# Performance work log

Measured on AMD Instinct MI355X. Metric: run time of the kernel, lower is better.

The kernel has to match this reference:

```python
import jax, jax.numpy as jnp
import numpy as np

N_NODES = 100000
N_EDGES = 1600000
N_GRAPHS = 1024
IN_CH = 64
HID = 32
H4, H2 = HID * 4, HID * 2


def _glorot(key, shape):
    fan_in, fan_out = shape[0], shape[1]
    lim = (6.0 / (fan_in + fan_out)) ** 0.5
    return jax.random.uniform(key, shape, jnp.float32, -lim, lim)


def setup_inputs() -> dict:
    key = jax.random.key(0)
    ks = jax.random.split(key, 32)
    inp = {
        "x": jax.random.normal(ks[0], (N_NODES, IN_CH), jnp.float32),
        "edge_index": jax.random.randint(ks[1], (2, N_EDGES), 0, N_NODES, jnp.int64),
        "batch": jnp.sort(jax.random.randint(ks[2], (N_NODES,), 0, N_GRAPHS, jnp.int64)),
    }
    dims = [(IN_CH, H4), (H4, H2), (H2, H2), (H2, H2)]
    for i, (di, do) in enumerate(dims, 1):
        inp[f"c{i}_wl"] = _glorot(ks[3 * i], (di, do))
        inp[f"c{i}_bl"] = jnp.zeros((do,), jnp.float32)
        inp[f"c{i}_wr"] = _glorot(ks[3 * i + 1], (di, do))
    lin_dims = [(H2, H2), (H2, HID), (HID, HID), (HID, 1)]
    for i, (di, do) in enumerate(lin_dims, 1):
        inp[f"lin{i}_w"] = _glorot(ks[15 + 2 * i], (di, do))
        inp[f"lin{i}_b"] = jnp.zeros((do,), jnp.float32)
    return inp


def _sage(x, src, dst, wl, bl, wr):
    # mean-aggregate neighbor (source) features at target nodes
    agg = jax.ops.segment_sum(x[src], dst, num_segments=N_NODES)
    deg = jax.ops.segment_sum(jnp.ones((src.shape[0],), x.dtype), dst, num_segments=N_NODES)
    agg = agg / jnp.maximum(deg, 1.0)[:, None]
    return agg @ wl + bl + x @ wr


def reference(x, edge_index, batch,
              c1_wl, c1_bl, c1_wr, c2_wl, c2_bl, c2_wr,
              c3_wl, c3_bl, c3_wr, c4_wl, c4_bl, c4_wr,
              lin1_w, lin1_b, lin2_w, lin2_b, lin3_w, lin3_b, lin4_w, lin4_b):
    src, dst = edge_index[0], edge_index[1]
    h = jax.nn.relu(_sage(x, src, dst, c1_wl, c1_bl, c1_wr))
    h = jax.nn.relu(_sage(h, src, dst, c2_wl, c2_bl, c2_wr))
    h = jax.nn.relu(_sage(h, src, dst, c3_wl, c3_bl, c3_wr))
    h = jax.nn.relu(_sage(h, src, dst, c4_wl, c4_bl, c4_wr))
    # global mean pool over graphs
    gsum = jax.ops.segment_sum(h, batch, num_segments=N_GRAPHS)
    gcnt = jax.ops.segment_sum(jnp.ones((h.shape[0],), h.dtype), batch, num_segments=N_GRAPHS)
    g = gsum / jnp.maximum(gcnt, 1.0)[:, None]
    g = jax.nn.relu(g @ lin1_w + lin1_b)
    g = jax.nn.relu(g @ lin2_w + lin2_b)
    g = jax.nn.relu(g @ lin3_w + lin3_b)
    out = (g @ lin4_w + lin4_b).squeeze(1)  # [N_GRAPHS]
    return out
```

## Files before the change

kernel.cpp:

```cpp
#include <hip/hip_runtime.h>

#define NN 100000
#define NE 1600000
#define NG 1024
#define CPAD 4
#define MAXDEG 64

#define GB_COUNT 6250
#define GB_Z     1563
#define GB_CVT   3125
#define GB_BND   5
#define GB_PREP  320
#define GB_ODD   (GB_Z + GB_CVT + GB_BND + GB_PREP)
#define GB_SETUP 12504

typedef __attribute__((ext_vector_type(8))) short bf16x8;
typedef __attribute__((ext_vector_type(4))) float f32x4;

__device__ __forceinline__ unsigned f2bf1(float f) {
  union { float f; unsigned u; } v; v.f = f;
  return (v.u + 0x7fffu + ((v.u >> 16) & 1u)) >> 16;
}
__device__ __forceinline__ unsigned packbf2(float a, float b) {
  return f2bf1(a) | (f2bf1(b) << 16);
}
__device__ __forceinline__ float bflo(unsigned u) {
  union { unsigned u; float f; } v; v.u = u << 16; return v.f;
}
__device__ __forceinline__ float bfhi(unsigned u) {
  union { unsigned u; float f; } v; v.u = u & 0xffff0000u; return v.f;
}
__device__ __forceinline__ float bfs(unsigned short s) {
  union { unsigned u; float f; } v; v.u = ((unsigned)s) << 16; return v.f;
}

#define ACC16(A, P0, P1)                                              \
  A[0] += bflo(P0.x); A[1] += bfhi(P0.x);                             \
  A[2] += bflo(P0.y); A[3] += bfhi(P0.y);                             \
  A[4] += bflo(P0.z); A[5] += bfhi(P0.z);                             \
  A[6] += bflo(P0.w); A[7] += bfhi(P0.w);                             \
  A[8] += bflo(P1.x); A[9] += bfhi(P1.x);                             \
  A[10] += bflo(P1.y); A[11] += bfhi(P1.y);                           \
  A[12] += bflo(P1.z); A[13] += bfhi(P1.z);                           \
  A[14] += bflo(P1.w); A[15] += bfhi(P1.w);

#define ACC8(A, V)                                                    \
  A[0] += bflo(V.x); A[1] += bfhi(V.x);                               \
  A[2] += bflo(V.y); A[3] += bfhi(V.y);                               \
  A[4] += bflo(V.z); A[5] += bfhi(V.z);                               \
  A[6] += bflo(V.w); A[7] += bfhi(V.w);

__global__ __launch_bounds__(256) void k_prepz(const float* __restrict__ c1wr,
                                               unsigned short* __restrict__ pLZ) {
  int e = blockIdx.x * 256 + threadIdx.x;
  if (e >= 64 * 128) return;
  int k = e >> 7, n = e & 127;
  int t = k >> 5, kq = (k >> 3) & 3, j = k & 7;
  int n0 = n >> 4, nl = n & 15;
  pLZ[((((n0 * 2 + t) * 64) + (kq * 16 + nl)) << 3) + j] =
      (unsigned short)f2bf1(c1wr[k * 128 + n]);
}

__global__ __launch_bounds__(256) void k_setup(
    const int* __restrict__ src, const int* __restrict__ dst,
    int* __restrict__ cnt, int* __restrict__ csr,
    const float* __restrict__ X, unsigned short* __restrict__ Xb,
    const int* __restrict__ batch, int* __restrict__ gstart,
    const unsigned short* __restrict__ pLZ, const float* __restrict__ c1bl,
    unsigned short* __restrict__ ZZ,
    const float* __restrict__ c1wl, const float* __restrict__ c1wr,
    const float* __restrict__ c2wl, const float* __restrict__ c2wr,
    const float* __restrict__ c3wl, const float* __restrict__ c3wr,
    const float* __restrict__ c4wl, const float* __restrict__ c4wr,
    unsigned short* __restrict__ pL1, unsigned short* __restrict__ pL2a,
    unsigned short* __restrict__ pL2b, unsigned short* __restrict__ pL3,
    unsigned short* __restrict__ pL4) {
  __shared__ __align__(16) char smem[64 * 66 * 4];
  int b = blockIdx.x, tid = threadIdx.x;
  int g = b >> 3, i = b & 7;

  if ((g & 1) == 0) {
    int cb = (g >> 1) * 8 + i;
    if (cb >= GB_COUNT) return;
    int e = cb * 256 + tid;
    int d = dst[e];
    int s = src[e];
    int r = atomicAdd(&cnt[(size_t)d * CPAD], 1);
    if (r < MAXDEG) csr[d * MAXDEG + r] = s;
    return;
  }
  int ob = (g >> 1) * 8 + i;
  if (ob >= GB_ODD) return;

  if (ob < GB_Z) {
    unsigned short* sA = (unsigned short*)smem;
    float* sC = (float*)smem;
    const int m0 = ob * 64;
#pragma unroll
    for (int l = 0; l < 2; ++l) {
      int c = tid + l * 256;
      int m = c >> 3, k8 = c & 7;
      int row = m0 + m;
      uint4 o = make_uint4(0, 0, 0, 0);
      if (row < NN) {
        const float4* xp = (const float4*)(X + (size_t)row * 64 + k8 * 8);
        float4 p0 = xp[0], p1 = xp[1];
        o.x = packbf2(p0.x, p0.y); o.y = packbf2(p0.z, p0.w);
        o.z = packbf2(p1.x, p1.y); o.w = packbf2(p1.z, p1.w);
      }
      int wv = m >> 4, mr = m & 15, t = k8 >> 2, kq = k8 & 3;
      ((uint4*)sA)[(wv * 2 + t) * 64 + kq * 16 + mr] = o;
    }
    __syncthreads();
    const int w = tid >> 6, L = tid & 63;
    const bf16x8* Af = (const bf16x8*)sA;
    const bf16x8* Bf = (const bf16x8*)pLZ;
    f32x4 acc[8];
#pragma unroll
    for (int i2 = 0; i2 < 8; ++i2)
#pragma unroll
      for (int j = 0; j < 4; ++j) acc[i2][j] = 0.f;
#pragma unroll
    for (int t = 0; t < 2; ++t) {
      bf16x8 afr = Af[(w * 2 + t) * 64 + L];
#pragma unroll
      for (int n0 = 0; n0 < 8; ++n0) {
        bf16x8 bfr = Bf[(n0 * 2 + t) * 64 + L];
        acc[n0] = __builtin_amdgcn_mfma_f32_16x16x32_bf16(afr, bfr, acc[n0], 0, 0, 0);
      }
    }
    int rg = L >> 4, cl = L & 15;
#pragma unroll
    for (int half = 0; half < 2; ++half) {
      __syncthreads();
#pragma unroll
      for (int n0 = 0; n0 < 4; ++n0)
#pragma unroll
        for (int r = 0; r < 4; ++r)
          sC[(w * 16 + rg * 4 + r) * 66 + n0 * 16 + cl] = acc[half * 4 + n0][r];
      __syncthreads();
#pragma unroll
      for (int it = 0; it < 2; ++it) {
        int c = tid + it * 256;
        int m = c >> 3, c8 = c & 7;
        int row = m0 + m;
        if (row < NN) {
          float v[8];
#pragma unroll
          for (int j = 0; j < 8; ++j)
            v[j] = sC[m * 66 + c8 * 8 + j] + c1bl[half * 64 + c8 * 8 + j];
          uint4 o;
          o.x = packbf2(v[0], v[1]); o.y = packbf2(v[2], v[3]);
          o.z = packbf2(v[4], v[5]); o.w = packbf2(v[6], v[7]);
          ((uint4*)(ZZ + (size_t)row * 128 + half * 64))[c8] = o;
        }
      }
    }
    return;
  }
  ob -= GB_Z;
  if (ob < GB_CVT) {
    int i2 = ob * 256 + tid;
    const float4* p = (const float4*)X + (size_t)i2 * 2;
    float4 a = p[0], c = p[1];
    uint4 o;
    o.x = packbf2(a.x, a.y); o.y = packbf2(a.z, a.w);
    o.z = packbf2(c.x, c.y); o.w = packbf2(c.z, c.w);
    ((uint4*)Xb)[i2] = o;
    return;
  }
  ob -= GB_CVT;
  if (ob < GB_BND) {
    int gg = ob * 256 + tid;
    if (gg > NG) return;
    int lo = 0, hi = NN;
    while (lo < hi) {
      int mid = (lo + hi) >> 1;
      if (batch[mid] < gg) lo = mid + 1; else hi = mid;
    }
    gstart[gg] = lo;
    return;
  }
  ob -= GB_BND;
  if (ob < GB_PREP) {
    int yb = ob >> 6, xb = ob & 63;
    const float *WL, *WR; unsigned short* dstp; int N;
    if (yb == 0)      { WL = c1wl; WR = c1wr;           dstp = pL1;  N = 128; }
    else if (yb == 1) { WL = c2wl; WR = c2wl + 64 * 64; dstp = pL2a; N = 64; }
    else if (yb == 2) { WL = c2wr; WR = c2wr + 64 * 64; dstp = pL2b; N = 64; }
    else if (yb == 3) { WL = c3wl; WR = c3wr;           dstp = pL3;  N = 64; }
    else              { WL = c4wl; WR = c4wr;           dstp = pL4;  N = 64; }
    int e = xb * 256 + tid;
    if (e >= 128 * N) return;
    int k = e / N, n = e - k * N;
    float w = (k < 64) ? WL[k * N + n] : WR[(k - 64) * N + n];
    int t = k >> 5, kq = (k >> 3) & 3, j = k & 7;
    int n0 = n >> 4, nl = n & 15;
    dstp[((((n0 * 4 + t) * 64) + (kq * 16 + nl)) << 3) + j] =
        (unsigned short)f2bf1(w);
  }
}

__global__ __launch_bounds__(256) void k_gather(
    const unsigned short* __restrict__ F, const int* __restrict__ csr,
    const int* __restrict__ cnt, const float* __restrict__ bias,
    const unsigned short* __restrict__ Z, unsigned short* __restrict__ out) {
  int idx = blockIdx.x * 256 + threadIdx.x;
  int n = idx >> 3, q = idx & 7;
  int deg = cnt[(size_t)n * CPAD];
  int degc = min(deg, MAXDEG);
  int beg = n * MAXDEG, end = beg + degc;
  float aA[8], aB[8];
#pragma unroll
  for (int c = 0; c < 8; ++c) { aA[c] = 0.f; aB[c] = 0.f; }
  int e = beg;
  for (; e + 8 <= end; e += 8) {
    int4 s0 = *(const int4*)(csr + e);
    int4 s1 = *(const int4*)(csr + e + 4);
    uint4 v0 = ((const uint4*)(F + (size_t)s0.x * 64))[q];
    uint4 v1 = ((const uint4*)(F + (size_t)s0.y * 64))[q];
    uint4 v2 = ((const uint4*)(F + (size_t)s0.z * 64))[q];
    uint4 v3 = ((const uint4*)(F + (size_t)s0.w * 64))[q];
    uint4 v4 = ((const uint4*)(F + (size_t)s1.x * 64))[q];
    uint4 v5 = ((const uint4*)(F + (size_t)s1.y * 64))[q];
    uint4 v6 = ((const uint4*)(F + (size_t)s1.z * 64))[q];
    uint4 v7 = ((const uint4*)(F + (size_t)s1.w * 64))[q];
    ACC8(aA, v0) ACC8(aB, v1) ACC8(aA, v2) ACC8(aB, v3)
    ACC8(aA, v4) ACC8(aB, v5) ACC8(aA, v6) ACC8(aB, v7)
  }
  if (e + 4 <= end) {
    int4 s0 = *(const int4*)(csr + e);
    uint4 v0 = ((const uint4*)(F + (size_t)s0.x * 64))[q];
    uint4 v1 = ((const uint4*)(F + (size_t)s0.y * 64))[q];
    uint4 v2 = ((const uint4*)(F + (size_t)s0.z * 64))[q];
    uint4 v3 = ((const uint4*)(F + (size_t)s0.w * 64))[q];
    ACC8(aA, v0) ACC8(aB, v1) ACC8(aA, v2) ACC8(aB, v3)
    e += 4;
  }
  for (; e < end; ++e) {
    uint4 v0 = ((const uint4*)(F + (size_t)csr[e] * 64))[q];
    ACC8(aA, v0)
  }
  float a[8];
  float iv = 1.0f / fmaxf((float)deg, 1.0f);
#pragma unroll
  for (int c = 0; c < 8; ++c) a[c] = (aA[c] + aB[c]) * iv;
  {
    uint4 z = ((const uint4*)(Z + (size_t)n * 64))[q];
    const float4* bp = (const float4*)(bias + q * 8);
    float4 b0 = bp[0], b1 = bp[1];
    a[0] = fmaxf(a[0] + b0.x + bflo(z.x), 0.f);
    a[1] = fmaxf(a[1] + b0.y + bfhi(z.x), 0.f);
    a[2] = fmaxf(a[2] + b0.z + bflo(z.y), 0.f);
    a[3] = fmaxf(a[3] + b0.w + bfhi(z.y), 0.f);
    a[4] = fmaxf(a[4] + b1.x + bflo(z.z), 0.f);
    a[5] = fmaxf(a[5] + b1.y + bfhi(z.z), 0.f);
    a[6] = fmaxf(a[6] + b1.z + bflo(z.w), 0.f);
    a[7] = fmaxf(a[7] + b1.w + bfhi(z.w), 0.f);
  }
  uint4 o;
  o.x = packbf2(a[0], a[1]); o.y = packbf2(a[2], a[3]);
  o.z = packbf2(a[4], a[5]); o.w = packbf2(a[6], a[7]);
  ((uint4*)(out + (size_t)n * 64))[q] = o;
}

__device__ __forceinline__ void gather_row(
    const unsigned short* __restrict__ F, const int* __restrict__ csr,
    const int* __restrict__ cnt, int row, int qr, float* a0) {
#pragma unroll
  for (int c = 0; c < 16; ++c) a0[c] = 0.f;
  int deg = cnt[(size_t)row * CPAD];
  int degc = min(deg, MAXDEG);
  int beg = row * MAXDEG, end = beg + degc;
  int e = beg;
  for (; e + 8 <= end; e += 8) {
    int4 sa = *(const int4*)(csr + e);
    int4 sb = *(const int4*)(csr + e + 4);
    const uint4* r0 = (const uint4*)(F + (size_t)sa.x * 64) + qr * 2;
    const uint4* r1 = (const uint4*)(F + (size_t)sa.y * 64) + qr * 2;
    const uint4* r2 = (const uint4*)(F + (size_t)sa.z * 64) + qr * 2;
    const uint4* r3 = (const uint4*)(F + (size_t)sa.w * 64) + qr * 2;
    const uint4* r4 = (const uint4*)(F + (size_t)sb.x * 64) + qr * 2;
    const uint4* r5 = (const uint4*)(F + (size_t)sb.y * 64) + qr * 2;
    const uint4* r6 = (const uint4*)(F + (size_t)sb.z * 64) + qr * 2;
    const uint4* r7 = (const uint4*)(F + (size_t)sb.w * 64) + qr * 2;
    uint4 p0 = r0[0], p1 = r0[1], p2 = r1[0], p3 = r1[1];
    uint4 p4 = r2[0], p5 = r2[1], p6 = r3[0], p7 = r3[1];
    uint4 q0 = r4[0], q1 = r4[1], q2 = r5[0], q3 = r5[1];
    uint4 q4 = r6[0], q5 = r6[1], q6 = r7[0], q7 = r7[1];
    ACC16(a0, p0, p1) ACC16(a0, p2, p3)
    ACC16(a0, p4, p5) ACC16(a0, p6, p7)
    ACC16(a0, q0, q1) ACC16(a0, q2, q3)
    ACC16(a0, q4, q5) ACC16(a0, q6, q7)
  }
  if (e + 4 <= end) {
    int4 sa = *(const int4*)(csr + e);
    const uint4* r0 = (const uint4*)(F + (size_t)sa.x * 64) + qr * 2;
    const uint4* r1 = (const uint4*)(F + (size_t)sa.y * 64) + qr * 2;
    const uint4* r2 = (const uint4*)(F + (size_t)sa.z * 64) + qr * 2;
    const uint4* r3 = (const uint4*)(F + (size_t)sa.w * 64) + qr * 2;
    uint4 p0 = r0[0], p1 = r0[1], p2 = r1[0], p3 = r1[1];
    uint4 p4 = r2[0], p5 = r2[1], p6 = r3[0], p7 = r3[1];
    ACC16(a0, p0, p1) ACC16(a0, p2, p3)
    ACC16(a0, p4, p5) ACC16(a0, p6, p7)
    e += 4;
  }
  if (e + 2 <= end) {
    int s0 = csr[e], s1 = csr[e + 1];
    const uint4* r0 = (const uint4*)(F + (size_t)s0 * 64) + qr * 2;
    const uint4* r1 = (const uint4*)(F + (size_t)s1 * 64) + qr * 2;
    uint4 p0 = r0[0], p1 = r0[1], q0 = r1[0], q1 = r1[1];
    ACC16(a0, p0, p1) ACC16(a0, q0, q1)
    e += 2;
  }
  if (e < end) {
    const uint4* r0 = (const uint4*)(F + (size_t)csr[e] * 64) + qr * 2;
    uint4 p0 = r0[0], p1 = r0[1];
    ACC16(a0, p0, p1)
  }
  float iv = 1.0f / fmaxf((float)deg, 1.0f);
#pragma unroll
  for (int c = 0; c < 16; ++c) a0[c] *= iv;
}

__global__ __launch_bounds__(256, 4) void k_fgemm1(
    const unsigned short* __restrict__ F, const int* __restrict__ csr,
    const int* __restrict__ cnt,
    const unsigned short* __restrict__ Wp,
    const unsigned short* __restrict__ ZZ,
    const unsigned short* __restrict__ Wa,
    const unsigned short* __restrict__ Wb,
    unsigned short* __restrict__ OUTa,
    unsigned short* __restrict__ OUTb) {
  __shared__ __align__(16) char smem[64 * 66 * 4 + 64 * 128 * 2];
  unsigned short* sA = (unsigned short*)smem;
  float* sC = (float*)smem;
  unsigned short* sA2 = (unsigned short*)(smem + 64 * 66 * 4);
  const int tid = threadIdx.x;
  const int m0 = blockIdx.x * 64;

  {
    int m = tid >> 2, qr = tid & 3;
    int row = m0 + m;
    float a0[16];
    if (row < NN) {
      gather_row(F, csr, cnt, row, qr, a0);
    } else {
#pragma unroll
      for (int c = 0; c < 16; ++c) a0[c] = 0.f;
    }
    int wv = m >> 4, mr = m & 15;
#pragma unroll
    for (int h = 0; h < 2; ++h) {
      int k8 = qr * 2 + h;
      int t = k8 >> 2, kq = k8 & 3;
      uint4 o;
      o.x = packbf2(a0[h * 8 + 0], a0[h * 8 + 1]);
      o.y = packbf2(a0[h * 8 + 2], a0[h * 8 + 3]);
      o.z = packbf2(a0[h * 8 + 4], a0[h * 8 + 5]);
      o.w = packbf2(a0[h * 8 + 6], a0[h * 8 + 7]);
      ((uint4*)sA)[(wv * 2 + t) * 64 + kq * 16 + mr] = o;
    }
  }
  __syncthreads();

  const int w = tid >> 6, L = tid & 63;
  const bf16x8* Af = (const bf16x8*)sA;
  const bf16x8* Bf = (const bf16x8*)Wp;
  f32x4 acc[8];
#pragma unroll
  for (int i = 0; i < 8; ++i)
#pragma unroll
    for (int j = 0; j < 4; ++j) acc[i][j] = 0.f;
#pragma unroll
  for (int t = 0; t < 2; ++t) {
    bf16x8 afr = Af[(w * 2 + t) * 64 + L];
#pragma unroll
    for (int n0 = 0; n0 < 8; ++n0) {
      bf16x8 bfr = Bf[(n0 * 4 + t) * 64 + L];
      acc[n0] = __builtin_amdgcn_mfma_f32_16x16x32_bf16(afr, bfr, acc[n0], 0, 0, 0);
    }
  }

  int rg = L >> 4, cl = L & 15;
#pragma unroll
  for (int half = 0; half < 2; ++half) {
    __syncthreads();
#pragma unroll
    for (int n0 = 0; n0 < 4; ++n0)
#pragma unroll
      for (int r = 0; r < 4; ++r)
        sC[(w * 16 + rg * 4 + r) * 66 + n0 * 16 + cl] = acc[half * 4 + n0][r];
    __syncthreads();
#pragma unroll
    for (int it = 0; it < 2; ++it) {
      int c = tid + it * 256;
      int m = c >> 3, c8 = c & 7;
      int row = m0 + m;
      uint4 o = make_uint4(0, 0, 0, 0);
      if (row < NN) {
        uint4 z = ((const uint4*)(ZZ + (size_t)row * 128 + half * 64))[c8];
        float zb[8] = {bflo(z.x), bfhi(z.x), bflo(z.y), bfhi(z.y),
                       bflo(z.z), bfhi(z.z), bflo(z.w), bfhi(z.w)};
        float v[8];
#pragma unroll
        for (int j = 0; j < 8; ++j)
          v[j] = fmaxf(sC[m * 66 + c8 * 8 + j] + zb[j], 0.f);
        o.x = packbf2(v[0], v[1]); o.y = packbf2(v[2], v[3]);
        o.z = packbf2(v[4], v[5]); o.w = packbf2(v[6], v[7]);
      }
      int k8 = half * 8 + c8, t = k8 >> 2, kq = k8 & 3;
      int wv = m >> 4, mr = m & 15;
      ((uint4*)sA2)[(wv * 4 + t) * 64 + kq * 16 + mr] = o;
    }
  }
  __syncthreads();

  const bf16x8* A2 = (const bf16x8*)sA2;
  const bf16x8* Ba = (const bf16x8*)Wa;
  const bf16x8* Bb = (const bf16x8*)Wb;
  f32x4 ca[4], cb[4];
#pragma unroll
  for (int i = 0; i < 4; ++i)
#pragma unroll
    for (int j = 0; j < 4; ++j) { ca[i][j] = 0.f; cb[i][j] = 0.f; }
#pragma unroll
  for (int t = 0; t < 4; ++t) {
    bf16x8 afr = A2[(w * 4 + t) * 64 + L];
#pragma unroll
    for (int n0 = 0; n0 < 4; ++n0) {
      ca[n0] = __builtin_amdgcn_mfma_f32_16x16x32_bf16(afr, Ba[(n0 * 4 + t) * 64 + L], ca[n0], 0, 0, 0);
      cb[n0] = __builtin_amdgcn_mfma_f32_16x16x32_bf16(afr, Bb[(n0 * 4 + t) * 64 + L], cb[n0], 0, 0, 0);
    }
  }
#pragma unroll
  for (int s = 0; s < 2; ++s) {
    unsigned short* OUT = s ? OUTb : OUTa;
    __syncthreads();
#pragma unroll
    for (int n0 = 0; n0 < 4; ++n0)
#pragma unroll
      for (int r = 0; r < 4; ++r)
        sC[(w * 16 + rg * 4 + r) * 66 + n0 * 16 + cl] =
            s ? cb[n0][r] : ca[n0][r];
    __syncthreads();
#pragma unroll
    for (int it = 0; it < 2; ++it) {
      int c = tid + it * 256;
      int m = c >> 3, c8 = c & 7;
      int row = m0 + m;
      if (row < NN) {
        float v[8];
#pragma unroll
        for (int j = 0; j < 8; ++j) v[j] = sC[m * 66 + c8 * 8 + j];
        uint4 o;
        o.x = packbf2(v[0], v[1]); o.y = packbf2(v[2], v[3]);
        o.z = packbf2(v[4], v[5]); o.w = packbf2(v[6], v[7]);
        ((uint4*)(OUT + (size_t)row * 64))[c8] = o;
      }
    }
  }
}

template <int NF>
__global__ __launch_bounds__(256, 4) void k_fgemm(
    const unsigned short* __restrict__ F, const int* __restrict__ csr,
    const int* __restrict__ cnt,
    const unsigned short* __restrict__ Wp, const float* __restrict__ bias,
    unsigned short* __restrict__ OUT, int outStride) {
  __shared__ __align__(16) char smem[64 * 66 * 4];
  unsigned short* sA = (unsigned short*)smem;
  float* sC = (float*)smem;
  const int tid = threadIdx.x;
  const int m0 = blockIdx.x * 64;

  {
    int m = tid >> 2, qr = tid & 3;
    int row = m0 + m;
    float a0[16];
    if (row < NN) {
      gather_row(F, csr, cnt, row, qr, a0);
    } else {
#pragma unroll
      for (int c = 0; c < 16; ++c) a0[c] = 0.f;
    }
    int wv = m >> 4, mr = m & 15;
#pragma unroll
    for (int h = 0; h < 2; ++h) {
      int k8 = qr * 2 + h;
      int t = k8 >> 2, kq = k8 & 3;
      uint4 o;
      o.x = packbf2(a0[h * 8 + 0], a0[h * 8 + 1]);
      o.y = packbf2(a0[h * 8 + 2], a0[h * 8 + 3]);
      o.z = packbf2(a0[h * 8 + 4], a0[h * 8 + 5]);
      o.w = packbf2(a0[h * 8 + 6], a0[h * 8 + 7]);
      ((uint4*)sA)[(wv * 4 + t) * 64 + kq * 16 + mr] = o;
    }
  }
#pragma unroll
  for (int l = 0; l < 2; ++l) {
    int c = tid + l * 256;
    int m = c >> 3, j = c & 7;
    int row = m0 + m;
    uint4 v = make_uint4(0, 0, 0, 0);
    if (row < NN) v = ((const uint4*)(F + (size_t)row * 64))[j];
    int k8 = 8 + j, t = k8 >> 2, kq = k8 & 3;
    int wv = m >> 4, mr = m & 15;
    ((uint4*)sA)[(wv * 4 + t) * 64 + kq * 16 + mr] = v;
  }
  __syncthreads();

  const int w = tid >> 6, L = tid & 63;
  const bf16x8* Af = (const bf16x8*)sA;
  const bf16x8* Bf = (const bf16x8*)Wp;
  f32x4 acc[NF];
#pragma unroll
  for (int i = 0; i < NF; ++i)
#pragma unroll
    for (int j = 0; j < 4; ++j) acc[i][j] = 0.f;
#pragma unroll
  for (int t = 0; t < 4; ++t) {
    bf16x8 afr = Af[(w * 4 + t) * 64 + L];
#pragma unroll
    for (int n0 = 0; n0 < NF; ++n0) {
      bf16x8 bfr = Bf[(n0 * 4 + t) * 64 + L];
      acc[n0] = __builtin_amdgcn_mfma_f32_16x16x32_bf16(afr, bfr, acc[n0], 0, 0, 0);
    }
  }

  int rg = L >> 4, cl = L & 15;
#pragma unroll
  for (int half = 0; half < NF / 4; ++half) {
    __syncthreads();
#pragma unroll
    for (int n0 = 0; n0 < 4; ++n0)
#pragma unroll
      for (int r = 0; r < 4; ++r)
        sC[(w * 16 + rg * 4 + r) * 66 + n0 * 16 + cl] = acc[half * 4 + n0][r];
    __syncthreads();
#pragma unroll
    for (int it = 0; it < 2; ++it) {
      int c = tid + it * 256;
      int m = c >> 3, c8 = c & 7;
      int row = m0 + m;
      if (row < NN) {
        float v[8];
#pragma unroll
        for (int j = 0; j < 8; ++j)
          v[j] = fmaxf(sC[m * 66 + c8 * 8 + j] + bias[half * 64 + c8 * 8 + j], 0.f);
        uint4 o;
        o.x = packbf2(v[0], v[1]); o.y = packbf2(v[2], v[3]);
        o.z = packbf2(v[4], v[5]); o.w = packbf2(v[6], v[7]);
        ((uint4*)(OUT + (size_t)row * outStride + half * 64))[c8] = o;
      }
    }
  }
}

__global__ __launch_bounds__(64) void k_poolmlp(
    const unsigned short* __restrict__ H, const int* __restrict__ gstart,
    const float* __restrict__ w1, const float* __restrict__ b1,
    const float* __restrict__ w2, const float* __restrict__ b2,
    const float* __restrict__ w3, const float* __restrict__ b3,
    const float* __restrict__ w4, const float* __restrict__ b4,
    float* __restrict__ out) {
  __shared__ float sg[64], s1[64], s2[32], s3[32];
  int g = blockIdx.x, t = threadIdx.x;
  int beg = gstart[g], end = gstart[g + 1];
  float a0 = 0.f, a1 = 0.f, a2 = 0.f, a3 = 0.f;
  int n = beg;
  for (; n + 4 <= end; n += 4) {
    a0 += bfs(H[(size_t)n * 64 + t]);
    a1 += bfs(H[(size_t)(n + 1) * 64 + t]);
    a2 += bfs(H[(size_t)(n + 2) * 64 + t]);
    a3 += bfs(H[(size_t)(n + 3) * 64 + t]);
  }
  for (; n < end; ++n) a0 += bfs(H[(size_t)n * 64 + t]);
  float cnt = fmaxf((float)(end - beg), 1.0f);
  sg[t] = ((a0 + a1) + (a2 + a3)) / cnt;
  __syncthreads();
  float acc = b1[t];
  for (int k = 0; k < 64; ++k) acc += sg[k] * w1[k * 64 + t];
  s1[t] = fmaxf(acc, 0.0f);
  __syncthreads();
  if (t < 32) {
    acc = b2[t];
    for (int k = 0; k < 64; ++k) acc += s1[k] * w2[k * 32 + t];
    s2[t] = fmaxf(acc, 0.0f);
  }
  __syncthreads();
  if (t < 32) {
    acc = b3[t];
    for (int k = 0; k < 32; ++k) acc += s2[k] * w3[k * 32 + t];
    s3[t] = fmaxf(acc, 0.0f);
  }
  __syncthreads();
  if (t == 0) {
    acc = b4[0];
    for (int k = 0; k < 32; ++k) acc += s3[k] * w4[k];
    out[g] = acc;
  }
}

extern "C" void kernel_launch(void* const* d_in, const int* in_sizes, int n_in,
                              void* d_out, int out_size, void* d_ws,
                              size_t ws_size, hipStream_t stream) {
  const float* x     = (const float*)d_in[0];
  const int*   ei    = (const int*)d_in[1];
  const int*   batch = (const int*)d_in[2];
  const int* src = ei;
  const int* dst = ei + NE;

  const float* c1_wl = (const float*)d_in[3];
  const float* c1_bl = (const float*)d_in[4];
  const float* c1_wr = (const float*)d_in[5];
  const float* c2_wl = (const float*)d_in[6];
  const float* c2_bl = (const float*)d_in[7];
  const float* c2_wr = (const float*)d_in[8];
  const float* c3_wl = (const float*)d_in[9];
  const float* c3_bl = (const float*)d_in[10];
  const float* c3_wr = (const float*)d_in[11];
  const float* c4_wl = (const float*)d_in[12];
  const float* c4_bl = (const float*)d_in[13];
  const float* c4_wr = (const float*)d_in[14];
  const float* l1w = (const float*)d_in[15];
  const float* l1b = (const float*)d_in[16];
  const float* l2w = (const float*)d_in[17];
  const float* l2b = (const float*)d_in[18];
  const float* l3w = (const float*)d_in[19];
  const float* l3b = (const float*)d_in[20];
  const float* l4w = (const float*)d_in[21];
  const float* l4b = (const float*)d_in[22];

  char* wsb = (char*)d_ws;
  unsigned short* xb  = (unsigned short*)wsb;
  unsigned short* B1  = xb + (size_t)NN * 64;
  unsigned short* B3  = B1 + (size_t)NN * 64;
  unsigned short* B4  = B3 + (size_t)NN * 64;
  unsigned short* ZZ  = B4 + (size_t)NN * 64;
  unsigned short* pL1  = ZZ + (size_t)NN * 128;
  unsigned short* pL2a = pL1 + 128 * 128;
  unsigned short* pL2b = pL2a + 128 * 64;
  unsigned short* pL3  = pL2b + 128 * 64;
  unsigned short* pL4  = pL3 + 128 * 64;
  unsigned short* pLZ  = pL4 + 128 * 64;
  int* cnt    = (int*)(pLZ + 64 * 128);
  int* gstart = cnt + (size_t)NN * CPAD;
  int* csr    = gstart + NG + 1 + 2;

  const int gN8 = NN * 8 / 256;
  const int gM  = (NN + 63) / 64;

  hipMemsetAsync(cnt, 0, (size_t)NN * CPAD * 4, stream);

  k_prepz<<<32, 256, 0, stream>>>(c1_wr, pLZ);

  k_setup<<<GB_SETUP, 256, 0, stream>>>(src, dst, cnt, csr, x, xb, batch,
                                        gstart, pLZ, c1_bl, ZZ,
                                        c1_wl, c1_wr, c2_wl, c2_wr,
                                        c3_wl, c3_wr, c4_wl, c4_wr,
                                        pL1, pL2a, pL2b, pL3, pL4);

  k_fgemm1<<<gM, 256, 0, stream>>>(xb, csr, cnt, pL1, ZZ, pL2a, pL2b, B3, B4);

  k_gather<<<gN8, 256, 0, stream>>>(B3, csr, cnt, c2_bl, B4, B1);

  k_fgemm<4><<<gM, 256, 0, stream>>>(B1, csr, cnt, pL3, c3_bl, B3, 64);

  k_fgemm<4><<<gM, 256, 0, stream>>>(B3, csr, cnt, pL4, c4_bl, B1, 64);

  k_poolmlp<<<NG, 64, 0, stream>>>(B1, gstart, l1w, l1b, l2w, l2b,
                                   l3w, l3b, l4w, l4b, (float*)d_out);
}
```

Baseline: 351.8 us.

## Sort rows by degree within tile for balanced gathers; fuse X bf16 conversion

Each fused gather+GEMM block now bitonic-sorts its 64 rows by in-degree in shared memory and assigns rows to threads in sorted order, so the threads in a wavefront have similar gather lengths and diverge less. The separate X-to-bf16 conversion blocks in setup are removed; the Z-GEMM blocks now write the bf16 X they already compute. The setup grid interleaving is rebalanced to 10 count groups per 3 other groups. The sort adds about 21 block-wide barriers per block and an extra indirection on the output rows.

```diff
diff --git a/kernel.cpp b/kernel.cpp
--- a/kernel.cpp
+++ b/kernel.cpp
@@ -8,11 +8,10 @@
 
 #define GB_COUNT 6250
 #define GB_Z     1563
-#define GB_CVT   3125
 #define GB_BND   5
 #define GB_PREP  320
-#define GB_ODD   (GB_Z + GB_CVT + GB_BND + GB_PREP)
-#define GB_SETUP 12504
+#define GB_ODD   (GB_Z + GB_BND + GB_PREP)
+#define GB_SETUP (79 * 13 * 8)
 
 typedef __attribute__((ext_vector_type(8))) short bf16x8;
 typedef __attribute__((ext_vector_type(4))) float f32x4;
@@ -78,18 +77,19 @@
   __shared__ __align__(16) char smem[64 * 66 * 4];
   int b = blockIdx.x, tid = threadIdx.x;
   int g = b >> 3, i = b & 7;
-
-  if ((g & 1) == 0) {
-    int cb = (g >> 1) * 8 + i;
+  int p = g / 13, r = g - p * 13;
+
+  if (r < 10) {
+    int cb = (p * 10 + r) * 8 + i;
     if (cb >= GB_COUNT) return;
     int e = cb * 256 + tid;
     int d = dst[e];
     int s = src[e];
-    int r = atomicAdd(&cnt[(size_t)d * CPAD], 1);
-    if (r < MAXDEG) csr[d * MAXDEG + r] = s;
+    int rk = atomicAdd(&cnt[(size_t)d * CPAD], 1);
+    if (rk < MAXDEG) csr[d * MAXDEG + rk] = s;
     return;
   }
-  int ob = (g >> 1) * 8 + i;
+  int ob = (p * 3 + (r - 10)) * 8 + i;
   if (ob >= GB_ODD) return;
 
   if (ob < GB_Z) {
@@ -107,6 +107,7 @@
         float4 p0 = xp[0], p1 = xp[1];
         o.x = packbf2(p0.x, p0.y); o.y = packbf2(p0.z, p0.w);
         o.z = packbf2(p1.x, p1.y); o.w = packbf2(p1.z, p1.w);
+        ((uint4*)(Xb + (size_t)row * 64))[k8] = o;
       }
       int wv = m >> 4, mr = m & 15, t = k8 >> 2, kq = k8 & 3;
       ((uint4*)sA)[(wv * 2 + t) * 64 + kq * 16 + mr] = o;
@@ -136,8 +137,8 @@
 #pragma unroll
       for (int n0 = 0; n0 < 4; ++n0)
 #pragma unroll
-        for (int r = 0; r < 4; ++r)
-          sC[(w * 16 + rg * 4 + r) * 66 + n0 * 16 + cl] = acc[half * 4 + n0][r];
+        for (int rr = 0; rr < 4; ++rr)
+          sC[(w * 16 + rg * 4 + rr) * 66 + n0 * 16 + cl] = acc[half * 4 + n0][rr];
       __syncthreads();
 #pragma unroll
       for (int it = 0; it < 2; ++it) {
@@ -159,17 +160,6 @@
     return;
   }
   ob -= GB_Z;
-  if (ob < GB_CVT) {
-    int i2 = ob * 256 + tid;
-    const float4* p = (const float4*)X + (size_t)i2 * 2;
-    float4 a = p[0], c = p[1];
-    uint4 o;
-    o.x = packbf2(a.x, a.y); o.y = packbf2(a.z, a.w);
-    o.z = packbf2(c.x, c.y); o.w = packbf2(c.z, c.w);
-    ((uint4*)Xb)[i2] = o;
-    return;
-  }
-  ob -= GB_CVT;
   if (ob < GB_BND) {
     int gg = ob * 256 + tid;
     if (gg > NG) return;
@@ -183,14 +173,14 @@
   }
   ob -= GB_BND;
   if (ob < GB_PREP) {
-    int yb = ob >> 6, xb = ob & 63;
+    int yb = ob >> 6, xb2 = ob & 63;
     const float *WL, *WR; unsigned short* dstp; int N;
     if (yb == 0)      { WL = c1wl; WR = c1wr;           dstp = pL1;  N = 128; }
     else if (yb == 1) { WL = c2wl; WR = c2wl + 64 * 64; dstp = pL2a; N = 64; }
     else if (yb == 2) { WL = c2wr; WR = c2wr + 64 * 64; dstp = pL2b; N = 64; }
     else if (yb == 3) { WL = c3wl; WR = c3wr;           dstp = pL3;  N = 64; }
     else              { WL = c4wl; WR = c4wr;           dstp = pL4;  N = 64; }
-    int e = xb * 256 + tid;
+    int e = xb2 * 256 + tid;
     if (e >= 128 * N) return;
     int k = e / N, n = e - k * N;
     float w = (k < 64) ? WL[k * N + n] : WR[(k - 64) * N + n];
@@ -198,6 +188,30 @@
     int n0 = n >> 4, nl = n & 15;
     dstp[((((n0 * 4 + t) * 64) + (kq * 16 + nl)) << 3) + j] =
         (unsigned short)f2bf1(w);
+  }
+}
+
+__device__ __forceinline__ void sort_deg(const int* __restrict__ cnt, int m0,
+                                         int tid, short* skey) {
+  if (tid < 64) {
+    int row = m0 + tid;
+    int dg = 0;
+    if (row < NN) dg = min(cnt[(size_t)row * CPAD], MAXDEG);
+    skey[tid] = (short)((dg << 6) | tid);
+  }
+  __syncthreads();
+  for (int k = 2; k <= 64; k <<= 1) {
+    for (int j = k >> 1; j > 0; j >>= 1) {
+      if (tid < 64) {
+        int pp = tid ^ j;
+        if (pp > tid) {
+          short a = skey[tid], b = skey[pp];
+          bool up = ((tid & k) == 0);
+          if ((a > b) == up) { skey[tid] = b; skey[pp] = a; }
+        }
+      }
+      __syncthreads();
+    }
   }
 }
 
@@ -333,15 +347,18 @@
     unsigned short* __restrict__ OUTa,
     unsigned short* __restrict__ OUTb) {
   __shared__ __align__(16) char smem[64 * 66 * 4 + 64 * 128 * 2];
+  __shared__ short skey[64];
   unsigned short* sA = (unsigned short*)smem;
   float* sC = (float*)smem;
   unsigned short* sA2 = (unsigned short*)(smem + 64 * 66 * 4);
   const int tid = threadIdx.x;
   const int m0 = blockIdx.x * 64;
 
+  sort_deg(cnt, m0, tid, skey);
+
   {
     int m = tid >> 2, qr = tid & 3;
-    int row = m0 + m;
+    int row = m0 + (skey[m] & 63);
     float a0[16];
     if (row < NN) {
       gather_row(F, csr, cnt, row, qr, a0);
@@ -389,14 +406,14 @@
 #pragma unroll
     for (int n0 = 0; n0 < 4; ++n0)
 #pragma unroll
-      for (int r = 0; r < 4; ++r)
-        sC[(w * 16 + rg * 4 + r) * 66 + n0 * 16 + cl] = acc[half * 4 + n0][r];
+      for (int rr = 0; rr < 4; ++rr)
+        sC[(w * 16 + rg * 4 + rr) * 66 + n0 * 16 + cl] = acc[half * 4 + n0][rr];
     __syncthreads();
 #pragma unroll
     for (int it = 0; it < 2; ++it) {
       int c = tid + it * 256;
       int m = c >> 3, c8 = c & 7;
-      int row = m0 + m;
+      int row = m0 + (skey[m] & 63);
       uint4 o = make_uint4(0, 0, 0, 0);
       if (row < NN) {
         uint4 z = ((const uint4*)(ZZ + (size_t)row * 128 + half * 64))[c8];
@@ -440,15 +457,15 @@
 #pragma unroll
     for (int n0 = 0; n0 < 4; ++n0)
 #pragma unroll
-      for (int r = 0; r < 4; ++r)
-        sC[(w * 16 + rg * 4 + r) * 66 + n0 * 16 + cl] =
-            s ? cb[n0][r] : ca[n0][r];
+      for (int rr = 0; rr < 4; ++rr)
+        sC[(w * 16 + rg * 4 + rr) * 66 + n0 * 16 + cl] =
+            s ? cb[n0][rr] : ca[n0][rr];
     __syncthreads();
 #pragma unroll
     for (int it = 0; it < 2; ++it) {
       int c = tid + it * 256;
       int m = c >> 3, c8 = c & 7;
-      int row = m0 + m;
+      int row = m0 + (skey[m] & 63);
       if (row < NN) {
         float v[8];
 #pragma unroll
@@ -469,14 +486,17 @@
     const unsigned short* __restrict__ Wp, const float* __restrict__ bias,
     unsigned short* __restrict__ OUT, int outStride) {
   __shared__ __align__(16) char smem[64 * 66 * 4];
+  __shared__ short skey[64];
   unsigned short* sA = (unsigned short*)smem;
   float* sC = (float*)smem;
   const int tid = threadIdx.x;
   const int m0 = blockIdx.x * 64;
 
+  sort_deg(cnt, m0, tid, skey);
+
   {
     int m = tid >> 2, qr = tid & 3;
-    int row = m0 + m;
+    int row = m0 + (skey[m] & 63);
     float a0[16];
     if (row < NN) {
       gather_row(F, csr, cnt, row, qr, a0);
@@ -501,7 +521,7 @@
   for (int l = 0; l < 2; ++l) {
     int c = tid + l * 256;
     int m = c >> 3, j = c & 7;
-    int row = m0 + m;
+    int row = m0 + (skey[m] & 63);
     uint4 v = make_uint4(0, 0, 0, 0);
     if (row < NN) v = ((const uint4*)(F + (size_t)row * 64))[j];
     int k8 = 8 + j, t = k8 >> 2, kq = k8 & 3;
@@ -535,14 +555,14 @@
 #pragma unroll
     for (int n0 = 0; n0 < 4; ++n0)
 #pragma unroll
-      for (int r = 0; r < 4; ++r)
-        sC[(w * 16 + rg * 4 + r) * 66 + n0 * 16 + cl] = acc[half * 4 + n0][r];
+      for (int rr = 0; rr < 4; ++rr)
+        sC[(w * 16 + rg * 4 + rr) * 66 + n0 * 16 + cl] = acc[half * 4 + n0][rr];
     __syncthreads();
 #pragma unroll
     for (int it = 0; it < 2; ++it) {
       int c = tid + it * 256;
       int m = c >> 3, c8 = c & 7;
-      int row = m0 + m;
+      int row = m0 + (skey[m] & 63);
       if (row < NN) {
         float v[8];
 #pragma unroll
```

After: 391.0 us. +11.1%, slower.
